# Kernel optimization log

Measured on AMD Instinct MI355X. Metric: run time of the kernel, lower is better.

## Reference

```python
import jax, jax.numpy as jnp
import numpy as np

B, LINES, NREG, D, L, K, CATS = 256, 64, 64, 1024, 64, 16, 2
EPS = 1e-5

_idx = np.arange(K)
# modular digit-wise add / sub mixing tables: M[i,j,m] = 1 iff (i op j) mod K == m
M_ADD = jnp.asarray(((_idx[:, None] + _idx[None, :]) % K)[..., None] == _idx[None, None, :], dtype=jnp.float32)
M_SUB = jnp.asarray(((_idx[:, None] - _idx[None, :]) % K)[..., None] == _idx[None, None, :], dtype=jnp.float32)


def _ln(x, g, b):
    m = x.mean(-1, keepdims=True)
    v = ((x - m) ** 2).mean(-1, keepdims=True)
    return (x - m) / jnp.sqrt(v + EPS) * g + b


def setup_inputs() -> dict:
    key = jax.random.key(0)
    ks = jax.random.split(key, 12)
    p = jax.random.uniform(ks[0], (B, LINES, CATS))
    opcode_probs = p / p.sum(-1, keepdims=True)
    registers = jax.random.normal(ks[1], (B, NREG, D))
    k_write = jax.random.normal(ks[2], (B, LINES, D))
    q_read = jax.random.normal(ks[3], (B, LINES, 2, D))
    cond_distribution = jax.random.uniform(ks[4], (B, LINES, 4))
    gate = jax.random.uniform(ks[5], (B, LINES, 1))
    s = 0.02
    F = L * K
    return {
        'opcode_probs': opcode_probs, 'registers': registers, 'k_write': k_write,
        'q_read': q_read, 'cond_distribution': cond_distribution, 'gate': gate,
        'ln1_g': jnp.ones((D,)), 'ln1_b': jnp.zeros((D,)),
        'w1': jax.random.normal(ks[6], (D, F)) * s, 'b1': jnp.zeros((F,)),
        'ln2_g': jnp.ones((D,)), 'ln2_b': jnp.zeros((D,)),
        'w2': jax.random.normal(ks[7], (D, F)) * s, 'b2': jnp.zeros((F,)),
        'w_res': jax.random.normal(ks[8], (F, D)) * s, 'b_res': jnp.zeros((D,)),
        'lno_g': jnp.ones((D,)), 'lno_b': jnp.zeros((D,)),
    }


def reference(opcode_probs, registers, k_write, q_read, cond_distribution, gate,
              ln1_g, ln1_b, w1, b1, ln2_g, ln2_b, w2, b2, w_res, b_res, lno_g, lno_b):
    scale = 1.0 / jnp.sqrt(jnp.asarray(D, jnp.float32))

    def digit_op(x, y, M):
        # x,y: (b,l,k) digit distributions -> (b,l,k) modular arithmetic result
        return jnp.einsum('bli,blj,ijm->blm', x, y, M)

    def step(R, xs):
        prob, q, kw, g = xs  # (b,2) (b,2,d) (b,d) (b,1)
        # attention read of two operands from register memory
        attn = jax.nn.softmax(jnp.einsum('bqd,brd->bqr', q, R) * scale, axis=-1)
        op_s = jnp.einsum('bqr,brd->bqd', attn, R)
        x = jax.nn.softmax((_ln(op_s[:, 0], ln1_g, ln1_b) @ w1 + b1).reshape(-1, L, K), axis=-1)
        y = jax.nn.softmax((_ln(op_s[:, 1], ln2_g, ln2_b) @ w2 + b2).reshape(-1, L, K), axis=-1)
        outs = jnp.stack([digit_op(x, y, M_ADD), digit_op(x, y, M_SUB)], axis=1)  # (b,2,l,k)
        mix = jnp.einsum('bn,bnlk->blk', prob, outs).reshape(-1, L * K)
        value = _ln(mix @ w_res + b_res, lno_g, lno_b)  # (b,d)
        # attention write-back with gate
        w = jax.nn.softmax(jnp.einsum('bd,brd->br', kw, R) * scale, axis=-1)
        gw = (g * w)[..., None]  # (b,r,1)
        R = R * (1.0 - gw) + gw * value[:, None, :]
        return R, None

    xs = (jnp.moveaxis(opcode_probs, 1, 0), jnp.moveaxis(q_read, 1, 0),
          jnp.moveaxis(k_write, 1, 0), jnp.moveaxis(gate, 1, 0))
    R, _ = jax.lax.scan(step, registers, xs)
    return R
```

## Files before the change

kernel.cpp:

```cpp
#include <hip/hip_runtime.h>
#include <hip/hip_bf16.h>

#define BB 256
#define LINES 64
#define NREG 64
#define DD 1024
#define FF 1024

constexpr float EPS = 1e-5f;
constexpr float SCALE = 0.03125f;

typedef __bf16 bf16_t;
typedef bf16_t bf16x8 __attribute__((ext_vector_type(8)));
typedef unsigned short us16x8 __attribute__((ext_vector_type(8)));
typedef float f32x4 __attribute__((ext_vector_type(4)));
typedef unsigned u32x4v __attribute__((ext_vector_type(4)));
typedef unsigned long long u64;

#define WS_W1T   0u
#define WS_W2T   (2u << 20)
#define WS_WRT   (4u << 20)
#define WS_XNP   (6u << 20)
#define WS_MIXP  (7u << 20)
#define WS_GT    ((7u << 20) + (1u << 19))
#define WS_CTR   ((8u << 20) + (1u << 19))
#define WS_XCDC  (WS_CTR + 1024u)
#define WS_NEED  (WS_XCDC + 64u)

#define SM_WV    0
#define SM_AT0P  256
#define SM_AT1P  512
#define SM_SC0   768
#define SM_SC1   1024
#define SM_SCW   1280
#define SM_RED   1536
#define SM_DYNID 1792
#define SM_DYN   2048
#define SM_OSB   SM_DYN
#define SM_AT0   SM_DYN
#define SM_AT1   (SM_DYN + 32768)
#define SM_RED2  (SM_DYN + 65536)
#define SM_PRE   (SM_DYN + 65536 + 13056)
#define SM_VAL   (SM_DYN + 65536 + 13056 + 8448)
#define SM_QPF   (SM_VAL + 4352)
#define SM_SIZE  (SM_QPF + 15360)

__device__ __forceinline__ float wred(float v) {
#pragma unroll
  for (int m = 32; m >= 1; m >>= 1) v += __shfl_xor(v, m);
  return v;
}
__device__ __forceinline__ float wmax64(float v) {
#pragma unroll
  for (int m = 32; m >= 1; m >>= 1) v = fmaxf(v, __shfl_xor(v, m));
  return v;
}

__device__ __forceinline__ void st_llc32(void* p, unsigned v) {
  asm volatile("global_store_dword %0, %1, off sc0 sc1" :: "v"(p), "v"(v) : "memory");
}
__device__ __forceinline__ void st_llc16b(void* p, unsigned short v) {
  unsigned vv = v;
  asm volatile("global_store_short %0, %1, off sc0 sc1" :: "v"(p), "v"(vv) : "memory");
}
__device__ __forceinline__ unsigned ld_llc32(const void* p) {
  unsigned r;
  asm volatile("global_load_dword %0, %1, off sc0 sc1\n\ts_waitcnt vmcnt(0)"
               : "=v"(r) : "v"(p) : "memory");
  return r;
}
__device__ __forceinline__ void ld_llc_4x8_nw(const void* p, u64& a, u64& b, u64& c, u64& d) {
  asm volatile(
      "global_load_dwordx2 %0, %4, off sc0 sc1\n\t"
      "global_load_dwordx2 %1, %4, off offset:8 sc0 sc1\n\t"
      "global_load_dwordx2 %2, %4, off offset:16 sc0 sc1\n\t"
      "global_load_dwordx2 %3, %4, off offset:24 sc0 sc1"
      : "=&v"(a), "=&v"(b), "=&v"(c), "=&v"(d) : "v"(p) : "memory");
}
__device__ __forceinline__ void ld_llc_16_nw(const void* p, u32x4v& r) {
  asm volatile("global_load_dwordx4 %0, %1, off sc0 sc1"
               : "=&v"(r) : "v"(p) : "memory");
}
__device__ __forceinline__ void wait_vm0() {
  asm volatile("s_waitcnt vmcnt(0)" ::: "memory");
  __builtin_amdgcn_sched_barrier(0);
}

__device__ __forceinline__ void group_barrier(unsigned* flg, int tid, int m, unsigned tag) {
  asm volatile("s_waitcnt vmcnt(0)" ::: "memory");
  __syncthreads();
  if (tid < 64) {
    if (tid == 0) st_llc32(&flg[m], tag);
    for (;;) {
      unsigned v = (tid < 16) ? ld_llc32(&flg[tid]) : tag;
      if (__all(v >= tag)) break;
      __builtin_amdgcn_s_sleep(2);
    }
  }
  __syncthreads();
}

__global__ __launch_bounds__(256) void transcvt(const float* __restrict__ w1,
                                                const float* __restrict__ w2,
                                                const float* __restrict__ wr,
                                                bf16_t* __restrict__ out) {
  __shared__ float tl[64][65];
  const float* src = (blockIdx.z == 0) ? w1 : (blockIdx.z == 1) ? w2 : wr;
  bf16_t* dst = out + (size_t)blockIdx.z * (1u << 20);
  const int i0 = blockIdx.x * 64, j0 = blockIdx.y * 64;
  const int t = threadIdx.x;
#pragma unroll
  for (int it = 0; it < 4; ++it) {
    int r = (t >> 4) + it * 16;
    int c4 = (t & 15) * 4;
    const float4 v = *reinterpret_cast<const float4*>(&src[(size_t)(i0 + r) * 1024 + j0 + c4]);
    tl[r][c4] = v.x; tl[r][c4 + 1] = v.y; tl[r][c4 + 2] = v.z; tl[r][c4 + 3] = v.w;
  }
  __syncthreads();
  const int orow = t >> 2, seg = t & 3;
  bf16x8 v0, v1;
#pragma unroll
  for (int u = 0; u < 8; ++u) {
    v0[u] = (bf16_t)tl[seg * 16 + u][orow];
    v1[u] = (bf16_t)tl[seg * 16 + 8 + u][orow];
  }
  bf16_t* dp = dst + (size_t)(j0 + orow) * 1024 + i0 + seg * 16;
  *reinterpret_cast<bf16x8*>(dp) = v0;
  *reinterpret_cast<bf16x8*>(dp + 8) = v1;
}

__global__ __launch_bounds__(1024, 4) void interp3(
    const float* __restrict__ opcode_probs, const float* __restrict__ Rin,
    const float* __restrict__ k_write, const float* __restrict__ q_read,
    const float* __restrict__ gate,
    const float* __restrict__ ln1_g, const float* __restrict__ ln1_b, const float* __restrict__ b1,
    const float* __restrict__ ln2_g, const float* __restrict__ ln2_b, const float* __restrict__ b2,
    const float* __restrict__ b_res, const float* __restrict__ lno_g, const float* __restrict__ lno_b,
    char* __restrict__ ws, float* __restrict__ Rout) {
  __shared__ __align__(16) char smem[SM_SIZE];
  float* wvp  = (float*)(smem + SM_WV);
  float* at0p = (float*)(smem + SM_AT0P);
  float* at1p = (float*)(smem + SM_AT1P);
  float* sc0p = (float*)(smem + SM_SC0);
  float* sc1p = (float*)(smem + SM_SC1);
  float* scwp = (float*)(smem + SM_SCW);
  float* redp = (float*)(smem + SM_RED);
  int*   dyn  = (int*)(smem + SM_DYNID);

  const int tid = threadIdx.x;
  const int w = tid >> 6, lane = tid & 63;
  const int ln15 = lane & 15, kgrp = lane >> 4;

  if (tid == 0) {
    unsigned x = __builtin_amdgcn_s_getreg(20 | (31 << 11)) & 7;
    unsigned r = atomicAdd((unsigned*)(ws + WS_XCDC) + x, 1u);
    dyn[0] = (int)x; dyn[1] = (int)r;
  }
  __syncthreads();
  const int xcd = dyn[0];
  const int rnk = dyn[1];
  const int g = (rnk >> 1) & 15;
  const int m = ((xcd << 1) | (rnk & 1)) & 15;
  const int j = m;
  const int bq = g * 16 + j;

  const bf16_t* w1t = (const bf16_t*)(ws + WS_W1T);
  const bf16_t* w2t = (const bf16_t*)(ws + WS_W2T);
  const bf16_t* wrt = (const bf16_t*)(ws + WS_WRT);
  unsigned* xnp   = (unsigned*)(ws + WS_XNP);
  bf16_t*  mixp   = (bf16_t*)(ws + WS_MIXP);
  unsigned* gtw   = (unsigned*)(ws + WS_GT);
  unsigned* flg   = (unsigned*)(ws + WS_CTR) + g * 16;

  float Rr_[4][16];
  {
    const float* Rsrc = Rin + (size_t)bq * (NREG * DD);
#pragma unroll
    for (int rr = 0; rr < 4; ++rr) {
#pragma unroll
      for (int c = 0; c < 4; ++c) {
        float4 v = *(const float4*)(Rsrc + (size_t)(4 * w + rr) * DD + lane * 16 + c * 4);
        Rr_[rr][c * 4 + 0] = v.x; Rr_[rr][c * 4 + 1] = v.y;
        Rr_[rr][c * 4 + 2] = v.z; Rr_[rr][c * 4 + 3] = v.w;
      }
    }
  }

  {
    const float* qb = q_read + ((size_t)bq * LINES + 0) * (2 * DD);
    const float* kb = k_write + ((size_t)bq * LINES + 0) * DD;
    float* qpf = (float*)(smem + SM_QPF);
    const int pidx = (tid >> 4) * 20 + (tid & 15);
    qpf[pidx] = qb[tid];
    qpf[1280 + pidx] = qb[DD + tid];
    qpf[2560 + pidx] = kb[tid];
  }
  __syncthreads();

  unsigned nbar = 0;

  for (int t = 0; t < LINES; ++t) {
    {
      const float* qpf = (const float*)(smem + SM_QPF);
      const int pb = lane * 20;
#pragma unroll
      for (int v = 0; v < 3; ++v) {
        float* dst = (v == 0) ? sc0p : (v == 1) ? sc1p : scwp;
        float qv[16];
#pragma unroll
        for (int c = 0; c < 4; ++c) {
          float4 t4 = *(const float4*)(qpf + v * 1280 + pb + c * 4);
          qv[c * 4 + 0] = t4.x; qv[c * 4 + 1] = t4.y;
          qv[c * 4 + 2] = t4.z; qv[c * 4 + 3] = t4.w;
        }
#pragma unroll
        for (int rr = 0; rr < 4; ++rr) {
          float s = 0.f;
#pragma unroll
          for (int jj = 0; jj < 16; ++jj) s = fmaf(Rr_[rr][jj], qv[jj], s);
          s = wred(s);
          if (lane == 0) dst[4 * w + rr] = s * SCALE;
        }
      }
    }
    __syncthreads();
    if (w < 3) {
      const float* src = (w == 0) ? sc0p : (w == 1) ? sc1p : scwp;
      float* dst = (w == 0) ? at0p : (w == 1) ? at1p : wvp;
      float v = src[lane];
      float mx = wmax64(v);
      float e = expf(v - mx);
      float s = wred(e);
      dst[lane] = e / s;
    }
    float pf0, pf1, pf2;
    {
      int tn = (t + 1 < LINES) ? (t + 1) : (LINES - 1);
      const float* qb2 = q_read + ((size_t)bq * LINES + tn) * (2 * DD);
      const float* kb2 = k_write + ((size_t)bq * LINES + tn) * DD;
      pf0 = qb2[tid]; pf1 = qb2[DD + tid]; pf2 = kb2[tid];
    }
    __syncthreads();
    float os0, os1;
    {
      float p0[16], p1[16];
#pragma unroll
      for (int jj = 0; jj < 16; ++jj) { p0[jj] = 0.f; p1[jj] = 0.f; }
#pragma unroll
      for (int rr = 0; rr < 4; ++rr) {
        float a0 = at0p[4 * w + rr], a1 = at1p[4 * w + rr];
#pragma unroll
        for (int jj = 0; jj < 16; ++jj) {
          p0[jj] = fmaf(a0, Rr_[rr][jj], p0[jj]);
          p1[jj] = fmaf(a1, Rr_[rr][jj], p1[jj]);
        }
      }
      float* osb = (float*)(smem + SM_OSB);
      const int rp = (tid >> 4) * 17 + (tid & 15);
#pragma unroll
      for (int jj = 0; jj < 16; ++jj) osb[w * 1088 + lane * 17 + jj] = p0[jj];
      __syncthreads();
      os0 = 0.f;
#pragma unroll
      for (int ww = 0; ww < 16; ++ww) os0 += osb[ww * 1088 + rp];
      __syncthreads();
#pragma unroll
      for (int jj = 0; jj < 16; ++jj) osb[w * 1088 + lane * 17 + jj] = p1[jj];
      __syncthreads();
      os1 = 0.f;
#pragma unroll
      for (int ww = 0; ww < 16; ++ww) os1 += osb[ww * 1088 + rp];
    }
    {
      float s0 = wred(os0), qq0 = wred(os0 * os0);
      float s1 = wred(os1), qq1 = wred(os1 * os1);
      if (lane == 0) { redp[w*4] = s0; redp[w*4+1] = qq0; redp[w*4+2] = s1; redp[w*4+3] = qq1; }
      __syncthreads();
      float S0 = 0, Q0 = 0, S1 = 0, Q1 = 0;
#pragma unroll
      for (int i = 0; i < 16; ++i) { S0 += redp[i*4]; Q0 += redp[i*4+1]; S1 += redp[i*4+2]; Q1 += redp[i*4+3]; }
      float m0 = S0 * (1.f / DD), v0 = fmaxf(Q0 * (1.f / DD) - m0 * m0, 0.f);
      float m1 = S1 * (1.f / DD), v1 = fmaxf(Q1 * (1.f / DD) - m1 * m1, 0.f);
      float xn0v = (os0 - m0) * rsqrtf(v0 + EPS) * ln1_g[tid] + ln1_b[tid];
      float xn1v = (os1 - m1) * rsqrtf(v1 + EPS) * ln2_g[tid] + ln2_b[tid];
      unsigned pw = (unsigned)__builtin_bit_cast(unsigned short, (bf16_t)xn0v)
                  | ((unsigned)__builtin_bit_cast(unsigned short, (bf16_t)xn1v) << 16);
      st_llc32(&xnp[((size_t)g * 16 + j) * DD + tid], pw);
    }
    group_barrier(flg, tid, m, ++nbar);

    {
      const char* base = (const char*)(xnp + (size_t)g * (16 * DD));
      const int row = tid >> 7, k16 = tid & 127;
      u64 a0, a1, a2, a3, c0, c1, c2, c3;
      ld_llc_4x8_nw(base + (size_t)row * 4096 + k16 * 32, a0, a1, a2, a3);
      ld_llc_4x8_nw(base + (size_t)(row + 8) * 4096 + k16 * 32, c0, c1, c2, c3);
      wait_vm0();
#pragma unroll
      for (int h = 0; h < 2; ++h) {
        u64 x0 = h ? c0 : a0, x1 = h ? c1 : a1, x2 = h ? c2 : a2, x3 = h ? c3 : a3;
        int r = row + h * 8;
        us16x8 v0, v1;
        v0[0] = (unsigned short)x0;         v1[0] = (unsigned short)(x0 >> 16);
        v0[1] = (unsigned short)(x0 >> 32); v1[1] = (unsigned short)(x0 >> 48);
        v0[2] = (unsigned short)x1;         v1[2] = (unsigned short)(x1 >> 16);
        v0[3] = (unsigned short)(x1 >> 32); v1[3] = (unsigned short)(x1 >> 48);
        v0[4] = (unsigned short)x2;         v1[4] = (unsigned short)(x2 >> 16);
        v0[5] = (unsigned short)(x2 >> 32); v1[5] = (unsigned short)(x2 >> 48);
        v0[6] = (unsigned short)x3;         v1[6] = (unsigned short)(x3 >> 16);
        v0[7] = (unsigned short)(x3 >> 32); v1[7] = (unsigned short)(x3 >> 48);
        unsigned byte = (unsigned)(r * 2048 + k16 * 16) ^ ((unsigned)(r & 7) << 4);
        *(us16x8*)(smem + SM_AT0 + byte) = v0;
        *(us16x8*)(smem + SM_AT1 + byte) = v1;
      }
    }
    __syncthreads();

#pragma unroll
    for (int gm = 0; gm < 2; ++gm) {
      const char* atile = smem + (gm ? SM_AT1 : SM_AT0);
      const int ns = w & 3, ks = w >> 2;
      const bf16_t* bsrc = (gm ? w2t : w1t) + (size_t)(64 * m + ns * 16 + ln15) * DD;
      f32x4 acc = {0.f, 0.f, 0.f, 0.f};
#pragma unroll
      for (int kc = 0; kc < 8; ++kc) {
        int kb = ks * 256 + kc * 32 + kgrp * 8;
        unsigned abyte = ((unsigned)(ln15 * 2048 + kb * 2)) ^ ((unsigned)(ln15 & 7) << 4);
        bf16x8 av = *(const bf16x8*)(atile + abyte);
        bf16x8 bv = *(const bf16x8*)(bsrc + kb);
        acc = __builtin_amdgcn_mfma_f32_16x16x32_bf16(av, bv, acc, 0, 0, 0);
      }
      float* red2 = (float*)(smem + SM_RED2);
      if (ks > 0) {
#pragma unroll
        for (int r2 = 0; r2 < 4; ++r2)
          red2[((ks - 1) * 4 + ns) * (16 * 17) + (kgrp * 4 + r2) * 17 + ln15] = acc[r2];
      }
      __syncthreads();
      if (ks == 0) {
        float* prep = (float*)(smem + SM_PRE) + gm * (16 * 66);
#pragma unroll
        for (int r2 = 0; r2 < 4; ++r2) {
          int crow = kgrp * 4 + r2;
          float v = acc[r2];
#pragma unroll
          for (int kk = 0; kk < 3; ++kk)
            v += red2[(kk * 4 + ns) * (16 * 17) + crow * 17 + ln15];
          prep[crow * 66 + ns * 16 + ln15] = v;
        }
      }
      __syncthreads();
    }
    {
      float* prep = (float*)(smem + SM_PRE);
      const int bb2 = w, c = lane;
      float xp = prep[bb2 * 66 + c] + b1[64 * m + c];
      float yp = prep[16 * 66 + bb2 * 66 + c] + b2[64 * m + c];
      float mx1 = xp, mx2 = yp;
#pragma unroll
      for (int msk = 1; msk < 16; msk <<= 1) {
        mx1 = fmaxf(mx1, __shfl_xor(mx1, msk));
        mx2 = fmaxf(mx2, __shfl_xor(mx2, msk));
      }
      float e1 = expf(xp - mx1), e2 = expf(yp - mx2);
      float s1 = e1, s2 = e2;
#pragma unroll
      for (int msk = 1; msk < 16; msk <<= 1) {
        s1 += __shfl_xor(s1, msk);
        s2 += __shfl_xor(s2, msk);
      }
      float x = e1 / s1, y = e2 / s2;
      int mm = lane & 15, basel = lane & ~15;
      float addv = 0.f, subv = 0.f;
#pragma unroll
      for (int i = 0; i < 16; ++i) {
        float xi = __shfl(x, basel + i);
        float ya = __shfl(y, basel + ((mm - i) & 15));
        float ys = __shfl(y, basel + ((i - mm) & 15));
        addv = fmaf(xi, ya, addv);
        subv = fmaf(xi, ys, subv);
      }
      int q2 = g * 16 + bb2;
      const float* pr = opcode_probs + ((size_t)q2 * LINES + t) * 2;
      float mix = pr[0] * addv + pr[1] * subv;
      st_llc16b(&mixp[((size_t)g * 16 + bb2) * DD + 64 * m + c],
                __builtin_bit_cast(unsigned short, (bf16_t)mix));
    }
    group_barrier(flg, tid, m, ++nbar);

    {
      const char* base = (const char*)(mixp + (size_t)g * (16 * DD));
      const int row = tid >> 7, k16 = tid & 127;
      u32x4v va, vb;
      ld_llc_16_nw(base + (size_t)row * 2048 + k16 * 16, va);
      ld_llc_16_nw(base + (size_t)(row + 8) * 2048 + k16 * 16, vb);
      wait_vm0();
      unsigned byte0 = (unsigned)(row * 2048 + k16 * 16) ^ ((unsigned)(row & 7) << 4);
      unsigned byte1 = (unsigned)((row + 8) * 2048 + k16 * 16) ^ ((unsigned)(row & 7) << 4);
      *(u32x4v*)(smem + SM_AT0 + byte0) = va;
      *(u32x4v*)(smem + SM_AT0 + byte1) = vb;
      __syncthreads();
      const int ns = w & 3, ks = w >> 2;
      const bf16_t* bsrc = wrt + (size_t)(64 * m + ns * 16 + ln15) * DD;
      f32x4 acc = {0.f, 0.f, 0.f, 0.f};
#pragma unroll
      for (int kc = 0; kc < 8; ++kc) {
        int kb = ks * 256 + kc * 32 + kgrp * 8;
        unsigned abyte = ((unsigned)(ln15 * 2048 + kb * 2)) ^ ((unsigned)(ln15 & 7) << 4);
        bf16x8 av = *(const bf16x8*)(smem + SM_AT0 + abyte);
        bf16x8 bv = *(const bf16x8*)(bsrc + kb);
        acc = __builtin_amdgcn_mfma_f32_16x16x32_bf16(av, bv, acc, 0, 0, 0);
      }
      float* red2 = (float*)(smem + SM_RED2);
      if (ks > 0) {
#pragma unroll
        for (int r2 = 0; r2 < 4; ++r2)
          red2[((ks - 1) * 4 + ns) * (16 * 17) + (kgrp * 4 + r2) * 17 + ln15] = acc[r2];
      }
      __syncthreads();
      if (ks == 0) {
        int f = 64 * m + ns * 16 + ln15;
#pragma unroll
        for (int r2 = 0; r2 < 4; ++r2) {
          int crow = kgrp * 4 + r2;
          float v = acc[r2];
#pragma unroll
          for (int kk = 0; kk < 3; ++kk)
            v += red2[(kk * 4 + ns) * (16 * 17) + crow * 17 + ln15];
          st_llc32(&gtw[((size_t)g * 16 + crow) * DD + f],
                   __builtin_bit_cast(unsigned, v + b_res[f]));
        }
      }
    }
    group_barrier(flg, tid, m, ++nbar);

    {
      float xv = __builtin_bit_cast(float, ld_llc32(&gtw[((size_t)g * 16 + j) * DD + tid]));
      float s1 = wred(xv), s2 = wred(xv * xv);
      if (lane == 0) { redp[w * 2] = s1; redp[w * 2 + 1] = s2; }
      __syncthreads();
      float S = 0.f, Q = 0.f;
#pragma unroll
      for (int i = 0; i < 16; ++i) { S += redp[i * 2]; Q += redp[i * 2 + 1]; }
      float mn = S * (1.f / DD), vr = fmaxf(Q * (1.f / DD) - mn * mn, 0.f);
      float vv = (xv - mn) * rsqrtf(vr + EPS) * lno_g[tid] + lno_b[tid];
      float* valp = (float*)(smem + SM_VAL);
      valp[(tid >> 4) * 17 + (tid & 15)] = vv;
    }
    __syncthreads();
    {
      float gtv = gate[(size_t)bq * LINES + t];
      const float* valp = (const float*)(smem + SM_VAL);
      float vvj[16];
#pragma unroll
      for (int jj = 0; jj < 16; ++jj) vvj[jj] = valp[lane * 17 + jj];
#pragma unroll
      for (int rr = 0; rr < 4; ++rr) {
        float gg = gtv * wvp[4 * w + rr];
#pragma unroll
        for (int jj = 0; jj < 16; ++jj)
          Rr_[rr][jj] = Rr_[rr][jj] * (1.f - gg) + gg * vvj[jj];
      }
      float* qpf = (float*)(smem + SM_QPF);
      const int pidx = (tid >> 4) * 20 + (tid & 15);
      qpf[pidx] = pf0;
      qpf[1280 + pidx] = pf1;
      qpf[2560 + pidx] = pf2;
    }
    __syncthreads();
  }

  {
    float* Rdst = Rout + (size_t)bq * (NREG * DD);
#pragma unroll
    for (int rr = 0; rr < 4; ++rr) {
#pragma unroll
      for (int c = 0; c < 4; ++c) {
        float4 v;
        v.x = Rr_[rr][c * 4 + 0]; v.y = Rr_[rr][c * 4 + 1];
        v.z = Rr_[rr][c * 4 + 2]; v.w = Rr_[rr][c * 4 + 3];
        *(float4*)(Rdst + (size_t)(4 * w + rr) * DD + lane * 16 + c * 4) = v;
      }
    }
  }
}

__global__ __launch_bounds__(1024) void interp_fb(
    const float* __restrict__ opcode_probs, const float* __restrict__ k_write,
    const float* __restrict__ q_read, const float* __restrict__ gate,
    const float* __restrict__ ln1_g, const float* __restrict__ ln1_b,
    const float* __restrict__ w1, const float* __restrict__ b1,
    const float* __restrict__ ln2_g, const float* __restrict__ ln2_b,
    const float* __restrict__ w2, const float* __restrict__ b2,
    const float* __restrict__ w_res, const float* __restrict__ b_res,
    const float* __restrict__ lno_g, const float* __restrict__ lno_b,
    float* __restrict__ R) {
  __shared__ float q0s[DD], q1s[DD], kws[DD];
  __shared__ float sc0[NREG], sc1[NREG], scw[NREG];
  __shared__ float at0[NREG], at1[NREG], wv[NREG];
  __shared__ float xn0[DD], xn1[DD];
  __shared__ float mixs[FF];
  __shared__ float val[DD];
  __shared__ float red[64];
  const int b = blockIdx.x;
  const int tid = threadIdx.x;
  const int w = tid >> 6, lane = tid & 63;
  float* Rb = R + (size_t)b * NREG * DD;
  for (int t = 0; t < LINES; ++t) {
    const float* qb = q_read + ((size_t)b * LINES + t) * 2 * DD;
    const float* kb = k_write + ((size_t)b * LINES + t) * DD;
    q0s[tid] = qb[tid]; q1s[tid] = qb[DD + tid]; kws[tid] = kb[tid];
    __syncthreads();
#pragma unroll
    for (int rr = 0; rr < 4; ++rr) {
      int r = w * 4 + rr;
      const float* Rr = Rb + (size_t)r * DD;
      float a0 = 0.f, a1 = 0.f, aw = 0.f;
#pragma unroll
      for (int jj = 0; jj < 16; ++jj) {
        int d = jj * 64 + lane;
        float rv = Rr[d];
        a0 += rv * q0s[d]; a1 += rv * q1s[d]; aw += rv * kws[d];
      }
      a0 = wred(a0); a1 = wred(a1); aw = wred(aw);
      if (lane == 0) { sc0[r] = a0 * SCALE; sc1[r] = a1 * SCALE; scw[r] = aw * SCALE; }
    }
    __syncthreads();
    if (w < 3) {
      const float* src = (w == 0) ? sc0 : (w == 1) ? sc1 : scw;
      float* dst = (w == 0) ? at0 : (w == 1) ? at1 : wv;
      float v = src[lane];
      float mx = wmax64(v);
      float e = expf(v - mx);
      float s = wred(e);
      dst[lane] = e / s;
    }
    __syncthreads();
    float os0 = 0.f, os1 = 0.f;
#pragma unroll 4
    for (int r = 0; r < NREG; ++r) {
      float rv = Rb[(size_t)r * DD + tid];
      os0 += at0[r] * rv; os1 += at1[r] * rv;
    }
    {
      float s0 = wred(os0), qq0 = wred(os0 * os0);
      float s1 = wred(os1), qq1 = wred(os1 * os1);
      if (lane == 0) { red[w*4] = s0; red[w*4+1] = qq0; red[w*4+2] = s1; red[w*4+3] = qq1; }
      __syncthreads();
      float S0 = 0, Q0 = 0, S1 = 0, Q1 = 0;
#pragma unroll
      for (int i = 0; i < 16; ++i) { S0 += red[i*4]; Q0 += red[i*4+1]; S1 += red[i*4+2]; Q1 += red[i*4+3]; }
      float m0 = S0 / DD, v0 = fmaxf(Q0 / DD - m0 * m0, 0.f);
      float m1 = S1 / DD, v1 = fmaxf(Q1 / DD - m1 * m1, 0.f);
      xn0[tid] = (os0 - m0) * rsqrtf(v0 + EPS) * ln1_g[tid] + ln1_b[tid];
      xn1[tid] = (os1 - m1) * rsqrtf(v1 + EPS) * ln2_g[tid] + ln2_b[tid];
      __syncthreads();
    }
    float p1v = b1[tid], p2v = b2[tid];
    {
      const float* c1 = w1 + tid;
      const float* c2 = w2 + tid;
#pragma unroll 4
      for (int d = 0; d < DD; ++d) {
        p1v += xn0[d] * c1[(size_t)d * FF];
        p2v += xn1[d] * c2[(size_t)d * FF];
      }
    }
    {
      int mmm = lane & 15, basel = lane & ~15;
      float mx1 = p1v, mx2 = p2v;
      for (int msk = 1; msk < 16; msk <<= 1) {
        mx1 = fmaxf(mx1, __shfl_xor(mx1, msk));
        mx2 = fmaxf(mx2, __shfl_xor(mx2, msk));
      }
      float e1 = expf(p1v - mx1), e2 = expf(p2v - mx2);
      float s1 = e1, s2 = e2;
      for (int msk = 1; msk < 16; msk <<= 1) { s1 += __shfl_xor(s1, msk); s2 += __shfl_xor(s2, msk); }
      float x = e1 / s1, y = e2 / s2;
      float addv = 0.f, subv = 0.f;
#pragma unroll
      for (int i = 0; i < 16; ++i) {
        float xi = __shfl(x, basel + i);
        float ya = __shfl(y, basel + ((mmm - i) & 15));
        float ys = __shfl(y, basel + ((i - mmm) & 15));
        addv += xi * ya; subv += xi * ys;
      }
      const float* pr = opcode_probs + ((size_t)b * LINES + t) * 2;
      mixs[tid] = pr[0] * addv + pr[1] * subv;
    }
    __syncthreads();
    float acc = b_res[tid];
    {
      const float* cr = w_res + tid;
#pragma unroll 4
      for (int f = 0; f < FF; ++f) acc += mixs[f] * cr[(size_t)f * DD];
    }
    {
      float s1 = wred(acc), s2 = wred(acc * acc);
      if (lane == 0) { red[w*2] = s1; red[w*2+1] = s2; }
      __syncthreads();
      float S = 0, Q = 0;
#pragma unroll
      for (int i = 0; i < 16; ++i) { S += red[i*2]; Q += red[i*2+1]; }
      float mn = S / DD, vr = fmaxf(Q / DD - mn * mn, 0.f);
      val[tid] = (acc - mn) * rsqrtf(vr + EPS) * lno_g[tid] + lno_b[tid];
      __syncthreads();
    }
    {
      float gt_ = gate[(size_t)b * LINES + t];
      float vv = val[tid];
#pragma unroll 4
      for (int r = 0; r < NREG; ++r) {
        float gg = gt_ * wv[r];
        size_t idx = (size_t)r * DD + tid;
        Rb[idx] = Rb[idx] * (1.f - gg) + gg * vv;
      }
    }
    __syncthreads();
  }
}

extern "C" void kernel_launch(void* const* d_in, const int* in_sizes, int n_in,
                              void* d_out, int out_size, void* d_ws, size_t ws_size,
                              hipStream_t stream) {
  const float* opcode = (const float*)d_in[0];
  const float* registers = (const float*)d_in[1];
  const float* k_write = (const float*)d_in[2];
  const float* q_read = (const float*)d_in[3];
  const float* gate = (const float*)d_in[5];
  const float* ln1_g = (const float*)d_in[6];
  const float* ln1_b = (const float*)d_in[7];
  const float* w1 = (const float*)d_in[8];
  const float* b1 = (const float*)d_in[9];
  const float* ln2_g = (const float*)d_in[10];
  const float* ln2_b = (const float*)d_in[11];
  const float* w2 = (const float*)d_in[12];
  const float* b2 = (const float*)d_in[13];
  const float* w_res = (const float*)d_in[14];
  const float* b_res = (const float*)d_in[15];
  const float* lno_g = (const float*)d_in[16];
  const float* lno_b = (const float*)d_in[17];
  float* R = (float*)d_out;

  if (ws_size >= (size_t)WS_NEED) {
    transcvt<<<dim3(16, 16, 3), 256, 0, stream>>>(w1, w2, w_res, (bf16_t*)d_ws);
    hipMemsetAsync((char*)d_ws + WS_CTR, 0, 2048, stream);
    interp3<<<BB, 1024, 0, stream>>>(opcode, registers, k_write, q_read, gate,
                                     ln1_g, ln1_b, b1, ln2_g, ln2_b, b2,
                                     b_res, lno_g, lno_b, (char*)d_ws, R);
  } else {
    hipMemcpyAsync(R, registers, (size_t)BB * NREG * DD * sizeof(float),
                   hipMemcpyDeviceToDevice, stream);
    interp_fb<<<BB, 1024, 0, stream>>>(opcode, k_write, q_read, gate, ln1_g, ln1_b,
                                       w1, b1, ln2_g, ln2_b, w2, b2, w_res, b_res,
                                       lno_g, lno_b, R);
  }
}
```

Before: 4.074 ms.

## Place each 16-block group on a single XCD and use L2-scope coherent accesses

Blocks now map to groups by XCD id, so each group of 16 cooperating blocks sits on one XCD. That makes it safe to drop the sc1 (system/LLC) bit on the exchange loads and stores and use sc0 (L2 scope) instead. The aim is to cut the latency of the intermediate activation exchanges between blocks in every step by serving them from the shared per-XCD L2 rather than the last-level cache. The scheme is only correct if every XCD receives exactly 32 blocks; an uneven dispatch would break group membership, and the barrier flags still use LLC-scope operations.

```diff
diff --git a/kernel.cpp b/kernel.cpp
--- a/kernel.cpp
+++ b/kernel.cpp
@@ -59,26 +59,36 @@
 __device__ __forceinline__ void st_llc32(void* p, unsigned v) {
   asm volatile("global_store_dword %0, %1, off sc0 sc1" :: "v"(p), "v"(v) : "memory");
 }
-__device__ __forceinline__ void st_llc16b(void* p, unsigned short v) {
-  unsigned vv = v;
-  asm volatile("global_store_short %0, %1, off sc0 sc1" :: "v"(p), "v"(vv) : "memory");
-}
 __device__ __forceinline__ unsigned ld_llc32(const void* p) {
   unsigned r;
   asm volatile("global_load_dword %0, %1, off sc0 sc1\n\ts_waitcnt vmcnt(0)"
                : "=v"(r) : "v"(p) : "memory");
   return r;
 }
-__device__ __forceinline__ void ld_llc_4x8_nw(const void* p, u64& a, u64& b, u64& c, u64& d) {
+
+__device__ __forceinline__ void st_l232(void* p, unsigned v) {
+  asm volatile("global_store_dword %0, %1, off sc0" :: "v"(p), "v"(v) : "memory");
+}
+__device__ __forceinline__ void st_l216b(void* p, unsigned short v) {
+  unsigned vv = v;
+  asm volatile("global_store_short %0, %1, off sc0" :: "v"(p), "v"(vv) : "memory");
+}
+__device__ __forceinline__ unsigned ld_l232(const void* p) {
+  unsigned r;
+  asm volatile("global_load_dword %0, %1, off sc0\n\ts_waitcnt vmcnt(0)"
+               : "=v"(r) : "v"(p) : "memory");
+  return r;
+}
+__device__ __forceinline__ void ld_l2_4x8_nw(const void* p, u64& a, u64& b, u64& c, u64& d) {
   asm volatile(
-      "global_load_dwordx2 %0, %4, off sc0 sc1\n\t"
-      "global_load_dwordx2 %1, %4, off offset:8 sc0 sc1\n\t"
-      "global_load_dwordx2 %2, %4, off offset:16 sc0 sc1\n\t"
-      "global_load_dwordx2 %3, %4, off offset:24 sc0 sc1"
+      "global_load_dwordx2 %0, %4, off sc0\n\t"
+      "global_load_dwordx2 %1, %4, off offset:8 sc0\n\t"
+      "global_load_dwordx2 %2, %4, off offset:16 sc0\n\t"
+      "global_load_dwordx2 %3, %4, off offset:24 sc0"
       : "=&v"(a), "=&v"(b), "=&v"(c), "=&v"(d) : "v"(p) : "memory");
 }
-__device__ __forceinline__ void ld_llc_16_nw(const void* p, u32x4v& r) {
-  asm volatile("global_load_dwordx4 %0, %1, off sc0 sc1"
+__device__ __forceinline__ void ld_l2_16_nw(const void* p, u32x4v& r) {
+  asm volatile("global_load_dwordx4 %0, %1, off sc0"
                : "=&v"(r) : "v"(p) : "memory");
 }
 __device__ __forceinline__ void wait_vm0() {
@@ -159,8 +169,8 @@
   __syncthreads();
   const int xcd = dyn[0];
   const int rnk = dyn[1];
-  const int g = (rnk >> 1) & 15;
-  const int m = ((xcd << 1) | (rnk & 1)) & 15;
+  const int g = ((xcd << 1) | ((rnk >> 4) & 1)) & 15;
+  const int m = rnk & 15;
   const int j = m;
   const int bq = g * 16 + j;
 
@@ -285,7 +295,7 @@
       float xn1v = (os1 - m1) * rsqrtf(v1 + EPS) * ln2_g[tid] + ln2_b[tid];
       unsigned pw = (unsigned)__builtin_bit_cast(unsigned short, (bf16_t)xn0v)
                   | ((unsigned)__builtin_bit_cast(unsigned short, (bf16_t)xn1v) << 16);
-      st_llc32(&xnp[((size_t)g * 16 + j) * DD + tid], pw);
+      st_l232(&xnp[((size_t)g * 16 + j) * DD + tid], pw);
     }
     group_barrier(flg, tid, m, ++nbar);
 
@@ -293,8 +303,8 @@
       const char* base = (const char*)(xnp + (size_t)g * (16 * DD));
       const int row = tid >> 7, k16 = tid & 127;
       u64 a0, a1, a2, a3, c0, c1, c2, c3;
-      ld_llc_4x8_nw(base + (size_t)row * 4096 + k16 * 32, a0, a1, a2, a3);
-      ld_llc_4x8_nw(base + (size_t)(row + 8) * 4096 + k16 * 32, c0, c1, c2, c3);
+      ld_l2_4x8_nw(base + (size_t)row * 4096 + k16 * 32, a0, a1, a2, a3);
+      ld_l2_4x8_nw(base + (size_t)(row + 8) * 4096 + k16 * 32, c0, c1, c2, c3);
       wait_vm0();
 #pragma unroll
       for (int h = 0; h < 2; ++h) {
@@ -383,8 +393,8 @@
       int q2 = g * 16 + bb2;
       const float* pr = opcode_probs + ((size_t)q2 * LINES + t) * 2;
       float mix = pr[0] * addv + pr[1] * subv;
-      st_llc16b(&mixp[((size_t)g * 16 + bb2) * DD + 64 * m + c],
-                __builtin_bit_cast(unsigned short, (bf16_t)mix));
+      st_l216b(&mixp[((size_t)g * 16 + bb2) * DD + 64 * m + c],
+               __builtin_bit_cast(unsigned short, (bf16_t)mix));
     }
     group_barrier(flg, tid, m, ++nbar);
 
@@ -392,8 +402,8 @@
       const char* base = (const char*)(mixp + (size_t)g * (16 * DD));
       const int row = tid >> 7, k16 = tid & 127;
       u32x4v va, vb;
-      ld_llc_16_nw(base + (size_t)row * 2048 + k16 * 16, va);
-      ld_llc_16_nw(base + (size_t)(row + 8) * 2048 + k16 * 16, vb);
+      ld_l2_16_nw(base + (size_t)row * 2048 + k16 * 16, va);
+      ld_l2_16_nw(base + (size_t)(row + 8) * 2048 + k16 * 16, vb);
       wait_vm0();
       unsigned byte0 = (unsigned)(row * 2048 + k16 * 16) ^ ((unsigned)(row & 7) << 4);
       unsigned byte1 = (unsigned)((row + 8) * 2048 + k16 * 16) ^ ((unsigned)(row & 7) << 4);
@@ -427,15 +437,15 @@
 #pragma unroll
           for (int kk = 0; kk < 3; ++kk)
             v += red2[(kk * 4 + ns) * (16 * 17) + crow * 17 + ln15];
-          st_llc32(&gtw[((size_t)g * 16 + crow) * DD + f],
-                   __builtin_bit_cast(unsigned, v + b_res[f]));
+          st_l232(&gtw[((size_t)g * 16 + crow) * DD + f],
+                  __builtin_bit_cast(unsigned, v + b_res[f]));
         }
       }
     }
     group_barrier(flg, tid, m, ++nbar);
 
     {
-      float xv = __builtin_bit_cast(float, ld_llc32(&gtw[((size_t)g * 16 + j) * DD + tid]));
+      float xv = __builtin_bit_cast(float, ld_l232(&gtw[((size_t)g * 16 + j) * DD + tid]));
       float s1 = wred(xv), s2 = wred(xv * xv);
       if (lane == 0) { redp[w * 2] = s1; redp[w * 2 + 1] = s2; }
       __syncthreads();
```

After: 4.147 ms. About the same (+1.8%).

## Fuse dual projection GEMMs, preload weights, add nt hints and move prefetch

Applied to the files above, without the earlier changes.

Merges the two per-operand MFMA GEMM loops into one loop that preloads both bf16 weight fragments into registers and issues interleaved MFMAs for x and y, with a doubled reduction scratch buffer. It raises wave priority around MFMA sections and adds nontemporal bits to cross-block exchange loads and stores, keeping separate flag helpers for the barrier. The next-step q/k prefetch is moved later, after the gather load, so that it stays off the critical attention phase. The register preload raises VGPR pressure, and the nt cache hints could change coherence or latency behaviour of the exchange traffic.

```diff
diff --git a/kernel.cpp b/kernel.cpp
--- a/kernel.cpp
+++ b/kernel.cpp
@@ -40,8 +40,8 @@
 #define SM_AT0   SM_DYN
 #define SM_AT1   (SM_DYN + 32768)
 #define SM_RED2  (SM_DYN + 65536)
-#define SM_PRE   (SM_DYN + 65536 + 13056)
-#define SM_VAL   (SM_DYN + 65536 + 13056 + 8448)
+#define SM_PRE   (SM_DYN + 65536 + 26112)
+#define SM_VAL   (SM_PRE + 8448)
 #define SM_QPF   (SM_VAL + 4352)
 #define SM_SIZE  (SM_QPF + 15360)
 
@@ -56,29 +56,39 @@
   return v;
 }
 
-__device__ __forceinline__ void st_llc32(void* p, unsigned v) {
+__device__ __forceinline__ void st_flag32(void* p, unsigned v) {
   asm volatile("global_store_dword %0, %1, off sc0 sc1" :: "v"(p), "v"(v) : "memory");
 }
-__device__ __forceinline__ void st_llc16b(void* p, unsigned short v) {
-  unsigned vv = v;
-  asm volatile("global_store_short %0, %1, off sc0 sc1" :: "v"(p), "v"(vv) : "memory");
-}
-__device__ __forceinline__ unsigned ld_llc32(const void* p) {
+__device__ __forceinline__ unsigned ld_flag32(const void* p) {
   unsigned r;
   asm volatile("global_load_dword %0, %1, off sc0 sc1\n\ts_waitcnt vmcnt(0)"
                : "=v"(r) : "v"(p) : "memory");
   return r;
 }
+
+__device__ __forceinline__ void st_llc32(void* p, unsigned v) {
+  asm volatile("global_store_dword %0, %1, off sc0 sc1 nt" :: "v"(p), "v"(v) : "memory");
+}
+__device__ __forceinline__ void st_llc16b(void* p, unsigned short v) {
+  unsigned vv = v;
+  asm volatile("global_store_short %0, %1, off sc0 sc1 nt" :: "v"(p), "v"(vv) : "memory");
+}
+__device__ __forceinline__ unsigned ld_llc32nt(const void* p) {
+  unsigned r;
+  asm volatile("global_load_dword %0, %1, off sc0 sc1 nt\n\ts_waitcnt vmcnt(0)"
+               : "=v"(r) : "v"(p) : "memory");
+  return r;
+}
 __device__ __forceinline__ void ld_llc_4x8_nw(const void* p, u64& a, u64& b, u64& c, u64& d) {
   asm volatile(
-      "global_load_dwordx2 %0, %4, off sc0 sc1\n\t"
-      "global_load_dwordx2 %1, %4, off offset:8 sc0 sc1\n\t"
-      "global_load_dwordx2 %2, %4, off offset:16 sc0 sc1\n\t"
-      "global_load_dwordx2 %3, %4, off offset:24 sc0 sc1"
+      "global_load_dwordx2 %0, %4, off sc0 sc1 nt\n\t"
+      "global_load_dwordx2 %1, %4, off offset:8 sc0 sc1 nt\n\t"
+      "global_load_dwordx2 %2, %4, off offset:16 sc0 sc1 nt\n\t"
+      "global_load_dwordx2 %3, %4, off offset:24 sc0 sc1 nt"
       : "=&v"(a), "=&v"(b), "=&v"(c), "=&v"(d) : "v"(p) : "memory");
 }
 __device__ __forceinline__ void ld_llc_16_nw(const void* p, u32x4v& r) {
-  asm volatile("global_load_dwordx4 %0, %1, off sc0 sc1"
+  asm volatile("global_load_dwordx4 %0, %1, off sc0 sc1 nt"
                : "=&v"(r) : "v"(p) : "memory");
 }
 __device__ __forceinline__ void wait_vm0() {
@@ -90,9 +100,9 @@
   asm volatile("s_waitcnt vmcnt(0)" ::: "memory");
   __syncthreads();
   if (tid < 64) {
-    if (tid == 0) st_llc32(&flg[m], tag);
+    if (tid == 0) st_flag32(&flg[m], tag);
     for (;;) {
-      unsigned v = (tid < 16) ? ld_llc32(&flg[tid]) : tag;
+      unsigned v = (tid < 16) ? ld_flag32(&flg[tid]) : tag;
       if (__all(v >= tag)) break;
       __builtin_amdgcn_s_sleep(2);
     }
@@ -200,6 +210,7 @@
   unsigned nbar = 0;
 
   for (int t = 0; t < LINES; ++t) {
+    float pf0, pf1, pf2;
     {
       const float* qpf = (const float*)(smem + SM_QPF);
       const int pb = lane * 20;
@@ -232,13 +243,6 @@
       float e = expf(v - mx);
       float s = wred(e);
       dst[lane] = e / s;
-    }
-    float pf0, pf1, pf2;
-    {
-      int tn = (t + 1 < LINES) ? (t + 1) : (LINES - 1);
-      const float* qb2 = q_read + ((size_t)bq * LINES + tn) * (2 * DD);
-      const float* kb2 = k_write + ((size_t)bq * LINES + tn) * DD;
-      pf0 = qb2[tid]; pf1 = qb2[DD + tid]; pf2 = kb2[tid];
     }
     __syncthreads();
     float os0, os1;
@@ -316,37 +320,51 @@
     }
     __syncthreads();
 
-#pragma unroll
-    for (int gm = 0; gm < 2; ++gm) {
-      const char* atile = smem + (gm ? SM_AT1 : SM_AT0);
+    {
       const int ns = w & 3, ks = w >> 2;
-      const bf16_t* bsrc = (gm ? w2t : w1t) + (size_t)(64 * m + ns * 16 + ln15) * DD;
-      f32x4 acc = {0.f, 0.f, 0.f, 0.f};
+      const bf16_t* b1p = w1t + (size_t)(64 * m + ns * 16 + ln15) * DD;
+      const bf16_t* b2p = w2t + (size_t)(64 * m + ns * 16 + ln15) * DD;
+      bf16x8 bva[8], bvb[8];
+#pragma unroll
+      for (int kc = 0; kc < 8; ++kc) {
+        int kb = ks * 256 + kc * 32 + kgrp * 8;
+        bva[kc] = *(const bf16x8*)(b1p + kb);
+        bvb[kc] = *(const bf16x8*)(b2p + kb);
+      }
+      f32x4 acc0 = {0.f, 0.f, 0.f, 0.f}, acc1 = {0.f, 0.f, 0.f, 0.f};
+      __builtin_amdgcn_s_setprio(1);
 #pragma unroll
       for (int kc = 0; kc < 8; ++kc) {
         int kb = ks * 256 + kc * 32 + kgrp * 8;
         unsigned abyte = ((unsigned)(ln15 * 2048 + kb * 2)) ^ ((unsigned)(ln15 & 7) << 4);
-        bf16x8 av = *(const bf16x8*)(atile + abyte);
-        bf16x8 bv = *(const bf16x8*)(bsrc + kb);
-        acc = __builtin_amdgcn_mfma_f32_16x16x32_bf16(av, bv, acc, 0, 0, 0);
-      }
+        bf16x8 av0 = *(const bf16x8*)(smem + SM_AT0 + abyte);
+        bf16x8 av1 = *(const bf16x8*)(smem + SM_AT1 + abyte);
+        acc0 = __builtin_amdgcn_mfma_f32_16x16x32_bf16(av0, bva[kc], acc0, 0, 0, 0);
+        acc1 = __builtin_amdgcn_mfma_f32_16x16x32_bf16(av1, bvb[kc], acc1, 0, 0, 0);
+      }
+      __builtin_amdgcn_s_setprio(0);
       float* red2 = (float*)(smem + SM_RED2);
       if (ks > 0) {
 #pragma unroll
-        for (int r2 = 0; r2 < 4; ++r2)
-          red2[((ks - 1) * 4 + ns) * (16 * 17) + (kgrp * 4 + r2) * 17 + ln15] = acc[r2];
+        for (int r2 = 0; r2 < 4; ++r2) {
+          red2[((0 * 3 + (ks - 1)) * 4 + ns) * (16 * 17) + (kgrp * 4 + r2) * 17 + ln15] = acc0[r2];
+          red2[((1 * 3 + (ks - 1)) * 4 + ns) * (16 * 17) + (kgrp * 4 + r2) * 17 + ln15] = acc1[r2];
+        }
       }
       __syncthreads();
       if (ks == 0) {
-        float* prep = (float*)(smem + SM_PRE) + gm * (16 * 66);
+        float* prep = (float*)(smem + SM_PRE);
 #pragma unroll
         for (int r2 = 0; r2 < 4; ++r2) {
           int crow = kgrp * 4 + r2;
-          float v = acc[r2];
-#pragma unroll
-          for (int kk = 0; kk < 3; ++kk)
-            v += red2[(kk * 4 + ns) * (16 * 17) + crow * 17 + ln15];
-          prep[crow * 66 + ns * 16 + ln15] = v;
+          float v0a = acc0[r2], v1a = acc1[r2];
+#pragma unroll
+          for (int kk = 0; kk < 3; ++kk) {
+            v0a += red2[((0 * 3 + kk) * 4 + ns) * (16 * 17) + crow * 17 + ln15];
+            v1a += red2[((1 * 3 + kk) * 4 + ns) * (16 * 17) + crow * 17 + ln15];
+          }
+          prep[crow * 66 + ns * 16 + ln15] = v0a;
+          prep[16 * 66 + crow * 66 + ns * 16 + ln15] = v1a;
         }
       }
       __syncthreads();
@@ -403,6 +421,7 @@
       const int ns = w & 3, ks = w >> 2;
       const bf16_t* bsrc = wrt + (size_t)(64 * m + ns * 16 + ln15) * DD;
       f32x4 acc = {0.f, 0.f, 0.f, 0.f};
+      __builtin_amdgcn_s_setprio(1);
 #pragma unroll
       for (int kc = 0; kc < 8; ++kc) {
         int kb = ks * 256 + kc * 32 + kgrp * 8;
@@ -411,6 +430,7 @@
         bf16x8 bv = *(const bf16x8*)(bsrc + kb);
         acc = __builtin_amdgcn_mfma_f32_16x16x32_bf16(av, bv, acc, 0, 0, 0);
       }
+      __builtin_amdgcn_s_setprio(0);
       float* red2 = (float*)(smem + SM_RED2);
       if (ks > 0) {
 #pragma unroll
@@ -435,7 +455,15 @@
     group_barrier(flg, tid, m, ++nbar);
 
     {
-      float xv = __builtin_bit_cast(float, ld_llc32(&gtw[((size_t)g * 16 + j) * DD + tid]));
+      float xv = __builtin_bit_cast(float, ld_llc32nt(&gtw[((size_t)g * 16 + j) * DD + tid]));
+      {
+        int tn = (t + 1 < LINES) ? (t + 1) : (LINES - 1);
+        const float* qb2 = q_read + ((size_t)bq * LINES + tn) * (2 * DD);
+        const float* kb2 = k_write + ((size_t)bq * LINES + tn) * DD;
+        pf0 = __builtin_nontemporal_load(qb2 + tid);
+        pf1 = __builtin_nontemporal_load(qb2 + DD + tid);
+        pf2 = __builtin_nontemporal_load(kb2 + tid);
+      }
       float s1 = wred(xv), s2 = wred(xv * xv);
       if (lane == 0) { redp[w * 2] = s1; redp[w * 2 + 1] = s2; }
       __syncthreads();
```

Result: slower. 4.319 ms (+6.0%).

## Split w_res GEMM over K per block with atomic accumulation, dropping a group barrier

Applied to the files above, without the earlier changes.

Each block now keeps its own 64-wide slice of the mix vector in shared memory and multiplies it against the matching K-slice of w_res for all 1024 outputs. The partial results are summed into a global buffer with float atomicAdd. This removes the global mix exchange and one cross-block group barrier per step, at the cost of many global atomics per step. The consumer now adds b_res, reads the sum, and resets the buffer to zero for the next step. Atomic accumulation makes the summation order nondeterministic, and the zero-reset ordering relies on the existing barriers.

```diff
diff --git a/kernel.cpp b/kernel.cpp
--- a/kernel.cpp
+++ b/kernel.cpp
@@ -14,14 +14,12 @@
 typedef bf16_t bf16x8 __attribute__((ext_vector_type(8)));
 typedef unsigned short us16x8 __attribute__((ext_vector_type(8)));
 typedef float f32x4 __attribute__((ext_vector_type(4)));
-typedef unsigned u32x4v __attribute__((ext_vector_type(4)));
 typedef unsigned long long u64;
 
 #define WS_W1T   0u
 #define WS_W2T   (2u << 20)
 #define WS_WRT   (4u << 20)
 #define WS_XNP   (6u << 20)
-#define WS_MIXP  (7u << 20)
 #define WS_GT    ((7u << 20) + (1u << 19))
 #define WS_CTR   ((8u << 20) + (1u << 19))
 #define WS_XCDC  (WS_CTR + 1024u)
@@ -43,7 +41,8 @@
 #define SM_PRE   (SM_DYN + 65536 + 13056)
 #define SM_VAL   (SM_DYN + 65536 + 13056 + 8448)
 #define SM_QPF   (SM_VAL + 4352)
-#define SM_SIZE  (SM_QPF + 15360)
+#define SM_MIXT  (SM_QPF + 15360)
+#define SM_SIZE  (SM_MIXT + 2304)
 
 __device__ __forceinline__ float wred(float v) {
 #pragma unroll
@@ -58,10 +57,6 @@
 
 __device__ __forceinline__ void st_llc32(void* p, unsigned v) {
   asm volatile("global_store_dword %0, %1, off sc0 sc1" :: "v"(p), "v"(v) : "memory");
-}
-__device__ __forceinline__ void st_llc16b(void* p, unsigned short v) {
-  unsigned vv = v;
-  asm volatile("global_store_short %0, %1, off sc0 sc1" :: "v"(p), "v"(vv) : "memory");
 }
 __device__ __forceinline__ unsigned ld_llc32(const void* p) {
   unsigned r;
@@ -76,10 +71,6 @@
       "global_load_dwordx2 %2, %4, off offset:16 sc0 sc1\n\t"
       "global_load_dwordx2 %3, %4, off offset:24 sc0 sc1"
       : "=&v"(a), "=&v"(b), "=&v"(c), "=&v"(d) : "v"(p) : "memory");
-}
-__device__ __forceinline__ void ld_llc_16_nw(const void* p, u32x4v& r) {
-  asm volatile("global_load_dwordx4 %0, %1, off sc0 sc1"
-               : "=&v"(r) : "v"(p) : "memory");
 }
 __device__ __forceinline__ void wait_vm0() {
   asm volatile("s_waitcnt vmcnt(0)" ::: "memory");
@@ -129,7 +120,7 @@
   *reinterpret_cast<bf16x8*>(dp + 8) = v1;
 }
 
-__global__ __launch_bounds__(1024, 4) void interp3(
+__global__ __launch_bounds__(1024, 4) void interp5(
     const float* __restrict__ opcode_probs, const float* __restrict__ Rin,
     const float* __restrict__ k_write, const float* __restrict__ q_read,
     const float* __restrict__ gate,
@@ -168,8 +159,8 @@
   const bf16_t* w2t = (const bf16_t*)(ws + WS_W2T);
   const bf16_t* wrt = (const bf16_t*)(ws + WS_WRT);
   unsigned* xnp   = (unsigned*)(ws + WS_XNP);
-  bf16_t*  mixp   = (bf16_t*)(ws + WS_MIXP);
-  unsigned* gtw   = (unsigned*)(ws + WS_GT);
+  float*    gtf   = (float*)(ws + WS_GT);
+  unsigned* gtu   = (unsigned*)(ws + WS_GT);
   unsigned* flg   = (unsigned*)(ws + WS_CTR) + g * 16;
 
   float Rr_[4][16];
@@ -383,59 +374,41 @@
       int q2 = g * 16 + bb2;
       const float* pr = opcode_probs + ((size_t)q2 * LINES + t) * 2;
       float mix = pr[0] * addv + pr[1] * subv;
-      st_llc16b(&mixp[((size_t)g * 16 + bb2) * DD + 64 * m + c],
-                __builtin_bit_cast(unsigned short, (bf16_t)mix));
-    }
-    group_barrier(flg, tid, m, ++nbar);
-
-    {
-      const char* base = (const char*)(mixp + (size_t)g * (16 * DD));
-      const int row = tid >> 7, k16 = tid & 127;
-      u32x4v va, vb;
-      ld_llc_16_nw(base + (size_t)row * 2048 + k16 * 16, va);
-      ld_llc_16_nw(base + (size_t)(row + 8) * 2048 + k16 * 16, vb);
-      wait_vm0();
-      unsigned byte0 = (unsigned)(row * 2048 + k16 * 16) ^ ((unsigned)(row & 7) << 4);
-      unsigned byte1 = (unsigned)((row + 8) * 2048 + k16 * 16) ^ ((unsigned)(row & 7) << 4);
-      *(u32x4v*)(smem + SM_AT0 + byte0) = va;
-      *(u32x4v*)(smem + SM_AT0 + byte1) = vb;
-      __syncthreads();
-      const int ns = w & 3, ks = w >> 2;
-      const bf16_t* bsrc = wrt + (size_t)(64 * m + ns * 16 + ln15) * DD;
-      f32x4 acc = {0.f, 0.f, 0.f, 0.f};
-#pragma unroll
-      for (int kc = 0; kc < 8; ++kc) {
-        int kb = ks * 256 + kc * 32 + kgrp * 8;
-        unsigned abyte = ((unsigned)(ln15 * 2048 + kb * 2)) ^ ((unsigned)(ln15 & 7) << 4);
-        bf16x8 av = *(const bf16x8*)(smem + SM_AT0 + abyte);
-        bf16x8 bv = *(const bf16x8*)(bsrc + kb);
-        acc = __builtin_amdgcn_mfma_f32_16x16x32_bf16(av, bv, acc, 0, 0, 0);
-      }
-      float* red2 = (float*)(smem + SM_RED2);
-      if (ks > 0) {
-#pragma unroll
-        for (int r2 = 0; r2 < 4; ++r2)
-          red2[((ks - 1) * 4 + ns) * (16 * 17) + (kgrp * 4 + r2) * 17 + ln15] = acc[r2];
-      }
-      __syncthreads();
-      if (ks == 0) {
-        int f = 64 * m + ns * 16 + ln15;
+      ((bf16_t*)(smem + SM_MIXT))[bb2 * 72 + c] = (bf16_t)mix;
+    }
+    __syncthreads();
+
+    {
+      const bf16_t* mixT = (const bf16_t*)(smem + SM_MIXT);
+      f32x4 acc[4] = {{0.f,0.f,0.f,0.f},{0.f,0.f,0.f,0.f},{0.f,0.f,0.f,0.f},{0.f,0.f,0.f,0.f}};
+#pragma unroll
+      for (int ks2 = 0; ks2 < 2; ++ks2) {
+        int fk = ks2 * 32 + kgrp * 8;
+        bf16x8 av = *(const bf16x8*)(mixT + ln15 * 72 + fk);
+#pragma unroll
+        for (int nt2 = 0; nt2 < 4; ++nt2) {
+          int d = 64 * w + nt2 * 16 + ln15;
+          const bf16_t* bp = wrt + (size_t)d * DD + 64 * m + fk;
+          bf16x8 bv = *(const bf16x8*)bp;
+          acc[nt2] = __builtin_amdgcn_mfma_f32_16x16x32_bf16(av, bv, acc[nt2], 0, 0, 0);
+        }
+      }
+#pragma unroll
+      for (int nt2 = 0; nt2 < 4; ++nt2) {
+        int d = 64 * w + nt2 * 16 + ln15;
 #pragma unroll
         for (int r2 = 0; r2 < 4; ++r2) {
           int crow = kgrp * 4 + r2;
-          float v = acc[r2];
-#pragma unroll
-          for (int kk = 0; kk < 3; ++kk)
-            v += red2[(kk * 4 + ns) * (16 * 17) + crow * 17 + ln15];
-          st_llc32(&gtw[((size_t)g * 16 + crow) * DD + f],
-                   __builtin_bit_cast(unsigned, v + b_res[f]));
+          atomicAdd(&gtf[((size_t)g * 16 + crow) * DD + d], acc[nt2][r2]);
         }
       }
     }
     group_barrier(flg, tid, m, ++nbar);
 
     {
-      float xv = __builtin_bit_cast(float, ld_llc32(&gtw[((size_t)g * 16 + j) * DD + tid]));
+      float xv = __builtin_bit_cast(float, ld_llc32(&gtu[((size_t)g * 16 + j) * DD + tid]))
+               + b_res[tid];
+      st_llc32(&gtu[((size_t)g * 16 + j) * DD + tid], 0u);
       float s1 = wred(xv), s2 = wred(xv * xv);
       if (lane == 0) { redp[w * 2] = s1; redp[w * 2 + 1] = s2; }
       __syncthreads();
@@ -644,8 +617,8 @@
 
   if (ws_size >= (size_t)WS_NEED) {
     transcvt<<<dim3(16, 16, 3), 256, 0, stream>>>(w1, w2, w_res, (bf16_t*)d_ws);
-    hipMemsetAsync((char*)d_ws + WS_CTR, 0, 2048, stream);
-    interp3<<<BB, 1024, 0, stream>>>(opcode, registers, k_write, q_read, gate,
+    hipMemsetAsync((char*)d_ws + WS_GT, 0, (1u << 20) + 2048, stream);
+    interp5<<<BB, 1024, 0, stream>>>(opcode, registers, k_write, q_read, gate,
                                      ln1_g, ln1_b, b1, ln2_g, ln2_b, b2,
                                      b_res, lno_g, lno_b, (char*)d_ws, R);
   } else {
```

Measured after the change: 4.126 ms. About the same (+1.3%).
